# Kernel tuning notes

Hardware: AMD Instinct MI355X
Metric: run time of the kernel (lower is better)

## Reference

```python
import jax, jax.numpy as jnp
import numpy as np

R = 2                                   # NMS radius (init kwarg r)
EPS = float(np.finfo(np.float32).eps)   # torch.finfo(float32).eps
PI = float(np.pi)


def _sobel(x):
    """Kornia SpatialGradient (sobel, normalized): x [N,1,H,W] -> (dx, dy) each [N,1,H,W]."""
    kx = jnp.array([[-1., 0., 1.], [-2., 0., 2.], [-1., 0., 1.]], jnp.float32) / 8.0
    ky = kx.T
    k = jnp.stack([kx, ky])[:, None]    # [2,1,3,3] -> out channels dx, dy
    xp = jnp.pad(x, ((0, 0), (0, 0), (1, 1), (1, 1)), mode='edge')  # replicate pad
    out = jax.lax.conv_general_dilated(xp, k, (1, 1), 'VALID',
                                       dimension_numbers=('NCHW', 'OIHW', 'NCHW'))
    return out[:, 0:1], out[:, 1:2]


def _theta(mask):
    """Edge direction from one-hot mask, per STEAL edges_nms. mask [N,1,H,W]."""
    dx, dy = _sobel(mask)
    gxx, _ = _sobel(dx)
    gxy, gyy = _sobel(dy)
    return jnp.fmod(jnp.arctan(gyy * jnp.sign(-gxy + EPS) / (gxx + EPS)), PI)


def setup_inputs() -> dict:
    key = jax.random.key(0)
    k1, k2 = jax.random.split(key)
    pred_labels = jax.random.normal(k1, (4, 16, 512, 1024), dtype=jnp.float32)
    true_labels = jax.random.randint(k2, (4, 512, 1024), 0, 16, dtype=jnp.int64)
    return {"pred_labels": pred_labels, "true_labels": true_labels}


def reference(pred_labels, true_labels):
    B, C, H, W = pred_labels.shape
    # per-class one-hot masks -> direction maps
    onehot = jax.nn.one_hot(true_labels, C, dtype=jnp.float32)        # [B,H,W,C]
    masks = onehot.transpose(0, 3, 1, 2).reshape(B * C, 1, H, W)
    theta = _theta(masks).reshape(B, C, H, W)
    thresh_theta = jnp.fmod(jnp.round(theta * (5.0 / PI)) + 5.0, 5.0)  # {0..4}
    dirs = jnp.fmod(thresh_theta, 4.0).astype(jnp.int32)               # {0,1,2,3}

    exp_p = jnp.exp(pred_labels)
    js = list(range(-R, R))
    # offsets (dx_off, dy_off) summed in the denominator for each direction
    offs = {
        0: [(0, j) for j in js],        # horizontal: preds[x, y-r:y+r]
        1: [(j, -j - 1) for j in js],   # anti-diagonal
        2: [(j, 0) for j in js],        # vertical: preds[x-r:x+r, y]
        3: [(-j - 1, j) for j in js],   # anti-diagonal (reversed traversal, same set)
    }
    denom = jnp.ones_like(exp_p)
    for d in range(4):
        dd = exp_p * 0.0
        for ox, oy in offs[d]:
            dd = dd + jnp.roll(exp_p, (-ox, -oy), axis=(2, 3))  # exp_p[x+ox, y+oy]
        denom = jnp.where(dirs == d, dd, denom)

    interior = jnp.zeros((H, W), bool).at[R:H - R, R:W - R].set(True)
    nms = jnp.where(interior, exp_p / denom, 0.0)
    return jnp.sum(nms)
```

## Files before the change

kernel.cpp:

```cpp
#include <hip/hip_runtime.h>


#define Bn 4
#define Cn 16
#define Hn 512
#define Wn 1024
#define TW 128
#define TH 32
#define LW 132
#define LH 36
#define NT 256

#define EPSF 1.1920928955078125e-07f
#define T1C 0.32491969623290623f
#define T2C 1.3763819204711735f

typedef unsigned long long u64;
typedef unsigned int u32;

static __device__ __forceinline__ float fast_rcp(float x) {
#if __has_builtin(__builtin_amdgcn_rcpf)
  return __builtin_amdgcn_rcpf(x);
#else
  return 1.0f / x;
#endif
}

__global__ __launch_bounds__(NT)
void steal_nms_kernel(const float* __restrict__ pred,
                      const int* __restrict__ labels,
                      float* __restrict__ out)
{
  __shared__ unsigned char labt[LH][LW];
  __shared__ float ext[LH][LW];
  __shared__ float wsum[NT/64];

  const int w0 = blockIdx.x * TW;
  const int h0 = blockIdx.y * TH;
  const int bz = blockIdx.z;
  const int b  = bz >> 4;
  const int c  = bz & 15;
  const int tid = threadIdx.x;

  for (int i = tid; i < LH * (LW/4); i += NT) {
    int row  = i / (LW/4);
    int col4 = (i - row*(LW/4)) * 4;
    int gh = h0 - 2 + row; gh = min(max(gh, 0), Hn-1);
    const int* lrow = labels + gh * Wn;
    u32 v = 0;
    #pragma unroll
    for (int k = 0; k < 4; ++k) {
      int gw = w0 - 2 + col4 + k; gw = min(max(gw, 0), Wn-1);
      v |= (u32)(lrow[gw] & 0xff) << (8*k);
    }
    *(u32*)&labt[row][col4] = v;
  }

  {
    const float* plane = pred + (size_t)(b*Cn + c) * (size_t)(Hn*Wn);
    for (int i = tid; i < LH*(LW/2); i += NT) {
      int row = i / (LW/2);
      int col = (i - row*(LW/2)) * 2;
      int gh = h0 - 2 + row; gh = min(max(gh, 0), Hn-1);
      int ga = w0 - 2 + col;
      int gb = ga + 1;
      ga = min(max(ga, 0), Wn-1);
      gb = min(max(gb, 0), Wn-1);
      const float* prow = plane + gh*Wn;
      float e0 = __expf(prow[ga]);
      float e1 = __expf(prow[gb]);
      *(float2*)&ext[row][col] = make_float2(e0, e1);
    }
  }
  __syncthreads();

  const int lane = tid & 63;
  const int wq   = tid >> 6;
  const int hr0  = wq * 8;

  u64 mm[12];
  {
    const int byte0 = 2*lane;
    const int j0 = byte0 >> 2;
    const int sh = (byte0 & 3) * 8;
    const u64 crep = 0x0101010101010101ULL * (u32)c;
    const u64 m80  = 0x8080808080808080ULL;
    #pragma unroll
    for (int r = 0; r < 12; ++r) {
      const u32* rowp = (const u32*)&labt[hr0 + r][0];
      u64 lo = rowp[j0];
      u64 hi = rowp[j0 + 1];
      u64 wvr = ((hi << 32) | lo) >> sh;
      u64 x = wvr ^ crep;
      mm[r] = ((m80 - x) & m80) >> 7;
    }
  }

  const int gw0 = w0 + 2*lane;
  const bool wvalid0 = (gw0     >= 2) && (gw0     < Wn-2);
  const bool wvalid1 = (gw0 + 1 >= 2) && (gw0 + 1 < Wn-2);

  float acc = 0.f;

  float exr[4][5];
  const int fb = 2*lane;
  #pragma unroll
  for (int r = 0; r < 3; ++r) {
    float2 p0 = *(const float2*)&ext[hr0 + r][fb];
    float2 p1 = *(const float2*)&ext[hr0 + r][fb + 2];
    exr[r][0] = p0.x; exr[r][1] = p0.y;
    exr[r][2] = p1.x; exr[r][3] = p1.y;
    exr[r][4] = ext[hr0 + r][fb + 4];
  }

  #pragma unroll
  for (int i = 0; i < 8; ++i) {
    {
      const int rn = (i + 3) & 3;
      float2 p0 = *(const float2*)&ext[hr0 + i + 3][fb];
      float2 p1 = *(const float2*)&ext[hr0 + i + 3][fb + 2];
      exr[rn][0] = p0.x; exr[rn][1] = p0.y;
      exr[rn][2] = p1.x; exr[rn][3] = p1.y;
      exr[rn][4] = ext[hr0 + i + 3][fb + 4];
    }

    u64 m0 = mm[i], m1 = mm[i+1], m2 = mm[i+2], m3 = mm[i+3], m4 = mm[i+4];
    u64 s13 = m1 + m3;
    u64 A  = m0 + m4 + (s13 << 2) + (m2 << 2) + (m2 << 1);
    u64 Bb = 0x0404040404040404ULL + (m3 << 1) + m4 - m0 - (m1 << 1);
    u64 Cb = 0x0404040404040404ULL + m0 + m4 - (m2 << 1);

    #define BY(x,k) ((int)((u32)((x) >> (8*(k))) & 0xffu))
    int A0=BY(A,0), A1=BY(A,1), A2=BY(A,2), A3=BY(A,3), A4=BY(A,4), A5=BY(A,5);
    int B0=BY(Bb,0), B1=BY(Bb,1), B2=BY(Bb,2), B3=BY(Bb,3), B4=BY(Bb,4), B5=BY(Bb,5);
    int C0=BY(Cb,0), C1=BY(Cb,1), C2=BY(Cb,2), C3=BY(Cb,3), C4=BY(Cb,4), C5=BY(Cb,5);
    #undef BY

    int gxx0 = A0 + A4 - 2*A2;
    int gxx1 = A1 + A5 - 2*A3;
    int gxyS0 = 2*(B3 - B1) + (B4 - B0);
    int gxyS1 = 2*(B4 - B2) + (B5 - B1);
    int gyy0 = C0 + C4 + 4*(C1 + C3) + 6*C2 - 64;
    int gyy1 = C1 + C5 + 4*(C2 + C4) + 6*C3 - 64;

    float den0 = fmaf((float)gxx0, 0.015625f, EPSF);
    float den1 = fmaf((float)gxx1, 0.015625f, EPSF);
    float gy0 = (float)gyy0 * 0.015625f;
    float gy1 = (float)gyy1 * 0.015625f;
    float num0 = (gxyS0 > 0) ? -gy0 : gy0;
    float num1 = (gxyS1 > 0) ? -gy1 : gy1;
    float an0 = fabsf(gy0), an1 = fabsf(gy1);
    float ad0 = fabsf(den0), ad1 = fabsf(den1);
    int rb0 = (int)(an0 >= T1C*ad0) + (int)(an0 >= T2C*ad0);
    int rb1 = (int)(an1 >= T1C*ad1) + (int)(an1 >= T2C*ad1);
    bool ng0 = ((__float_as_int(num0) ^ __float_as_int(den0)) < 0);
    bool ng1 = ((__float_as_int(num1) ^ __float_as_int(den1)) < 0);
    int dir0 = ng0 ? ((rb0 == 2) ? 3 : 0) : rb0;
    int dir1 = ng1 ? ((rb1 == 2) ? 3 : 0) : rb1;

    const float* r0 = exr[(i+0)&3];
    const float* r1 = exr[(i+1)&3];
    const float* r2 = exr[(i+2)&3];
    const float* r3 = exr[(i+3)&3];

    float t12 = r2[1] + r2[2];
    float D0a = t12 + r2[0] + r2[3];
    float D0b = t12 + r2[3] + r2[4];
    float D2a = (r0[2] + r1[2]) + (r2[2] + r3[2]);
    float D2b = (r0[3] + r1[3]) + (r2[3] + r3[3]);
    float Dda = (r0[3] + r1[2]) + (r2[1] + r3[0]);
    float Ddb = (r0[4] + r1[3]) + (r2[2] + r3[1]);

    float dena = (dir0 == 0) ? D0a : ((dir0 == 2) ? D2a : Dda);
    float denb = (dir1 == 0) ? D0b : ((dir1 == 2) ? D2b : Ddb);

    const int gh = h0 + hr0 + i;
    const bool hv = (gh >= 2) && (gh < Hn-2);
    float na = (hv && wvalid0) ? r2[2] : 0.f;
    float nb = (hv && wvalid1) ? r2[3] : 0.f;
    acc += na * fast_rcp(dena);
    acc += nb * fast_rcp(denb);
  }

  #pragma unroll
  for (int off = 32; off > 0; off >>= 1)
    acc += __shfl_down(acc, off);
  if (lane == 0) wsum[wq] = acc;
  __syncthreads();
  if (tid == 0) {
    float s = 0.f;
    #pragma unroll
    for (int q = 0; q < NT/64; ++q) s += wsum[q];
    atomicAdd(out, s);
  }
}

extern "C" void kernel_launch(void* const* d_in, const int* in_sizes, int n_in,
                              void* d_out, int out_size, void* d_ws, size_t ws_size,
                              hipStream_t stream) {
  (void)in_sizes; (void)n_in; (void)d_ws; (void)ws_size; (void)out_size;
  const float* pred   = (const float*)d_in[0];
  const int*   labels = (const int*)d_in[1];
  float* out = (float*)d_out;

  hipMemsetAsync(out, 0, sizeof(float), stream);

  dim3 grid(Wn/TW, Hn/TH, Bn*Cn);
  steal_nms_kernel<<<grid, NT, 0, stream>>>(pred, labels, out);
}
```

Baseline: 302.0 us.

## Halve tile height, vectorize interior tile loads, spread atomics over partial sums

```diff
diff --git a/kernel.cpp b/kernel.cpp
--- a/kernel.cpp
+++ b/kernel.cpp
@@ -6,9 +6,9 @@
 #define Hn 512
 #define Wn 1024
 #define TW 128
-#define TH 32
+#define TH 16
 #define LW 132
-#define LH 36
+#define LH 20
 #define NT 256
 
 #define EPSF 1.1920928955078125e-07f
@@ -17,6 +17,8 @@
 
 typedef unsigned long long u64;
 typedef unsigned int u32;
+typedef float f4u __attribute__((ext_vector_type(4), aligned(4)));
+typedef int   i4u __attribute__((ext_vector_type(4), aligned(4)));
 
 static __device__ __forceinline__ float fast_rcp(float x) {
 #if __has_builtin(__builtin_amdgcn_rcpf)
@@ -29,7 +31,7 @@
 __global__ __launch_bounds__(NT)
 void steal_nms_kernel(const float* __restrict__ pred,
                       const int* __restrict__ labels,
-                      float* __restrict__ out)
+                      float* __restrict__ ws)
 {
   __shared__ unsigned char labt[LH][LW];
   __shared__ float ext[LH][LW];
@@ -42,22 +44,38 @@
   const int c  = bz & 15;
   const int tid = threadIdx.x;
 
-  for (int i = tid; i < LH * (LW/4); i += NT) {
-    int row  = i / (LW/4);
-    int col4 = (i - row*(LW/4)) * 4;
-    int gh = h0 - 2 + row; gh = min(max(gh, 0), Hn-1);
-    const int* lrow = labels + gh * Wn;
-    u32 v = 0;
-    #pragma unroll
-    for (int k = 0; k < 4; ++k) {
-      int gw = w0 - 2 + col4 + k; gw = min(max(gw, 0), Wn-1);
-      v |= (u32)(lrow[gw] & 0xff) << (8*k);
-    }
-    *(u32*)&labt[row][col4] = v;
-  }
-
-  {
-    const float* plane = pred + (size_t)(b*Cn + c) * (size_t)(Hn*Wn);
+  const float* plane = pred + (size_t)(b*Cn + c) * (size_t)(Hn*Wn);
+  const bool interior = (h0 >= 2) && (h0 + TH + 2 <= Hn) &&
+                        (w0 >= 2) && (w0 + TW + 2 <= Wn);
+
+  if (interior) {
+    const int*   lb = labels + (size_t)(h0-2)*Wn + (w0-2);
+    const float* pb = plane  + (size_t)(h0-2)*Wn + (w0-2);
+    for (int i = tid; i < LH*33; i += NT) {
+      int row = i / 33;
+      int c4  = (i - row*33) * 4;
+      i4u L = *(const i4u*)(lb + row*Wn + c4);
+      u32 v = (u32)L.x | ((u32)L.y << 8) | ((u32)L.z << 16) | ((u32)L.w << 24);
+      *(u32*)&labt[row][c4] = v;
+      f4u p = *(const f4u*)(pb + row*Wn + c4);
+      float4 e;
+      e.x = __expf(p.x); e.y = __expf(p.y); e.z = __expf(p.z); e.w = __expf(p.w);
+      *(float4*)&ext[row][c4] = e;
+    }
+  } else {
+    for (int i = tid; i < LH * (LW/4); i += NT) {
+      int row  = i / (LW/4);
+      int col4 = (i - row*(LW/4)) * 4;
+      int gh = h0 - 2 + row; gh = min(max(gh, 0), Hn-1);
+      const int* lrow = labels + gh * Wn;
+      u32 v = 0;
+      #pragma unroll
+      for (int k = 0; k < 4; ++k) {
+        int gw = w0 - 2 + col4 + k; gw = min(max(gw, 0), Wn-1);
+        v |= (u32)(lrow[gw] & 0xff) << (8*k);
+      }
+      *(u32*)&labt[row][col4] = v;
+    }
     for (int i = tid; i < LH*(LW/2); i += NT) {
       int row = i / (LW/2);
       int col = (i - row*(LW/2)) * 2;
@@ -76,9 +94,9 @@
 
   const int lane = tid & 63;
   const int wq   = tid >> 6;
-  const int hr0  = wq * 8;
-
-  u64 mm[12];
+  const int hr0  = wq * 4;
+
+  u64 mm[TH/4 + 4];
   {
     const int byte0 = 2*lane;
     const int j0 = byte0 >> 2;
@@ -86,7 +104,7 @@
     const u64 crep = 0x0101010101010101ULL * (u32)c;
     const u64 m80  = 0x8080808080808080ULL;
     #pragma unroll
-    for (int r = 0; r < 12; ++r) {
+    for (int r = 0; r < TH/4 + 4; ++r) {
       const u32* rowp = (const u32*)&labt[hr0 + r][0];
       u64 lo = rowp[j0];
       u64 hi = rowp[j0 + 1];
@@ -114,7 +132,7 @@
   }
 
   #pragma unroll
-  for (int i = 0; i < 8; ++i) {
+  for (int i = 0; i < TH/4; ++i) {
     {
       const int rn = (i + 3) & 3;
       float2 p0 = *(const float2*)&ext[hr0 + i + 3][fb];
@@ -191,20 +209,33 @@
     float s = 0.f;
     #pragma unroll
     for (int q = 0; q < NT/64; ++q) s += wsum[q];
-    atomicAdd(out, s);
-  }
+    atomicAdd(&ws[(bz << 2) | (blockIdx.x & 3)], s);
+  }
+}
+
+__global__ __launch_bounds__(64)
+void reduce_ws_kernel(const float* __restrict__ ws, float* __restrict__ out)
+{
+  const int l = threadIdx.x;
+  float s = (ws[l] + ws[l + 64]) + (ws[l + 128] + ws[l + 192]);
+  #pragma unroll
+  for (int off = 32; off > 0; off >>= 1)
+    s += __shfl_down(s, off);
+  if (l == 0) *out = s;
 }
 
 extern "C" void kernel_launch(void* const* d_in, const int* in_sizes, int n_in,
                               void* d_out, int out_size, void* d_ws, size_t ws_size,
                               hipStream_t stream) {
-  (void)in_sizes; (void)n_in; (void)d_ws; (void)ws_size; (void)out_size;
+  (void)in_sizes; (void)n_in; (void)ws_size; (void)out_size;
   const float* pred   = (const float*)d_in[0];
   const int*   labels = (const int*)d_in[1];
   float* out = (float*)d_out;
-
-  hipMemsetAsync(out, 0, sizeof(float), stream);
+  float* ws  = (float*)d_ws;
+
+  hipMemsetAsync(ws, 0, 256 * sizeof(float), stream);
 
   dim3 grid(Wn/TW, Hn/TH, Bn*Cn);
-  steal_nms_kernel<<<grid, NT, 0, stream>>>(pred, labels, out);
-}
+  steal_nms_kernel<<<grid, NT, 0, stream>>>(pred, labels, ws);
+  reduce_ws_kernel<<<1, 64, 0, stream>>>(ws, out);
+}
```

Measured after the change: 265.4 us. 12.1% less time.
